# Kernel tuning notes

Measured on AMD Instinct MI355X. Metric: run time of the kernel, lower is better.

Reference implementation:

```python
import jax, jax.numpy as jnp
import numpy as np

B, S, E, H, L, DFF = 2, 2048, 512, 8, 2, 2048
D = E // H
EPS = 1e-5


def layernorm(x, g, b):
    mu = jnp.mean(x, axis=-1, keepdims=True)
    var = jnp.var(x, axis=-1, keepdims=True)
    return (x - mu) * jax.lax.rsqrt(var + EPS) * g + b


def layernorm_noaffine(x):
    mu = jnp.mean(x, axis=-1, keepdims=True)
    var = jnp.var(x, axis=-1, keepdims=True)
    return (x - mu) * jax.lax.rsqrt(var + EPS)


def setup_inputs() -> dict:
    key = jax.random.key(0)
    ks = jax.random.split(key, 16)
    s = 0.02
    inp = {
        "x": jax.random.normal(ks[0], (B, S, E), dtype=jnp.float32),
        "mask": jax.random.randint(ks[1], (B, S), 0, 2) == 1,
        # per-layer attention projections, stacked over layers
        "wq": jax.random.normal(ks[2], (L, E, E), dtype=jnp.float32) * s,
        "bq": jnp.zeros((L, E), dtype=jnp.float32),
        "wk": jax.random.normal(ks[3], (L, E, E), dtype=jnp.float32) * s,
        "bk": jnp.zeros((L, E), dtype=jnp.float32),
        "wv": jax.random.normal(ks[4], (L, E, E), dtype=jnp.float32) * s,
        "bv": jnp.zeros((L, E), dtype=jnp.float32),
        # shared norms (module defines a single norm1/norm2 used by every layer)
        "g1": jnp.ones((E,), dtype=jnp.float32),
        "b1": jnp.zeros((E,), dtype=jnp.float32),
        "g2": jnp.ones((E,), dtype=jnp.float32),
        "b2": jnp.zeros((E,), dtype=jnp.float32),
        "gf": jnp.ones((E,), dtype=jnp.float32),
        "bf": jnp.zeros((E,), dtype=jnp.float32),
        # shared Dense FFN (single self.dense used after every layer)
        "W1": jax.random.normal(ks[5], (DFF, E), dtype=jnp.float32) * s,
        "B1": jnp.zeros((DFF,), dtype=jnp.float32),
        "W2": jax.random.normal(ks[6], (E, DFF), dtype=jnp.float32) * s,
        "B2": jnp.zeros((E,), dtype=jnp.float32),
    }
    return inp


def _forward(x, wq, bq, wk, bk, wv, bv, g1, b1, g2, b2, gf, bf, W1, B1, W2, B2, mask):
    scale = 1.0 / jnp.sqrt(jnp.float32(D))
    m = mask[:, None, None, :]  # [B,1,1,S] key padding mask, True = pad
    neg_inf = jnp.float32(-jnp.inf)
    for i in range(L):
        h = layernorm(x, g1, b1)  # norm1(x), used for q,k,v
        q = (h @ wq[i].T + bq[i]).reshape(B, S, H, D).transpose(0, 2, 1, 3)
        k = (h @ wk[i].T + bk[i]).reshape(B, S, H, D).transpose(0, 2, 1, 3)
        v = (h @ wv[i].T + bv[i]).reshape(B, S, H, D).transpose(0, 2, 1, 3)
        logits = jnp.einsum("bhqd,bhkd->bhqk", q, k) * scale
        att = jax.nn.softmax(jnp.where(m, neg_inf, logits), axis=-1)
        att = jnp.where(m, 0.0, att)
        out = jnp.einsum("bhqk,bhkd->bhqd", att, v)
        out = out.transpose(0, 2, 1, 3).reshape(B, S, E)
        x = x + layernorm(out, g2, b2)
        # Dense: LayerNorm(no affine) -> Linear -> ReLU -> Linear, residual
        d = layernorm_noaffine(x)
        d = jax.nn.relu(d @ W1.T + B1)
        d = d @ W2.T + B2
        x = x + d
    return layernorm(x, gf, bf)


def reference(x, mask, wq, bq, wk, bk, wv, bv, g1, b1, g2, b2, gf, bf, W1, B1, W2, B2):
    return _forward(x, wq, bq, wk, bk, wv, bv, g1, b1, g2, b2, gf, bf, W1, B1, W2, B2, mask)
```

## Files before the change

kernel.cpp:

```cpp
#include <hip/hip_runtime.h>
#include <hip/hip_bf16.h>

constexpr int BB   = 2;
constexpr int SS   = 2048;
constexpr int EE   = 512;
constexpr int HH   = 8;
constexpr int DD   = 64;
constexpr int DFF_ = 2048;
constexpr int NTOK = BB * SS;
constexpr int NE   = NTOK * EE;
constexpr float EPSF  = 1e-5f;
constexpr float SCL2  = 0.125f * 1.44269504088896f;
constexpr float MBIAS = -1e30f;
constexpr int KSPLIT = 2;
constexpr int KHALF  = SS / KSPLIT;

typedef __bf16 v8bf __attribute__((ext_vector_type(8)));
typedef __bf16 v4bf __attribute__((ext_vector_type(4)));
typedef float  v4f  __attribute__((ext_vector_type(4)));

__device__ __forceinline__ float bf2f(unsigned short u) {
    return __uint_as_float(((unsigned int)u) << 16);
}
__device__ __forceinline__ float bf2f(__bf16 u) {
    unsigned short us = __builtin_bit_cast(unsigned short, u);
    return __uint_as_float(((unsigned int)us) << 16);
}
__device__ __forceinline__ float ldA(const void* p, size_t i, int f) {
    return f ? ((const float*)p)[i] : bf2f(((const unsigned short*)p)[i]);
}
__device__ __forceinline__ void gll16(const void* g, void* l) {
    __builtin_amdgcn_global_load_lds(
        (const __attribute__((address_space(1))) void*)g,
        (__attribute__((address_space(3))) void*)l, 16, 0, 0);
}

__global__ void sniff_kernel(const unsigned short* __restrict__ x, int* flag) {
    __shared__ int cnt[256];
    int t = threadIdx.x, bad = 0;
    for (int i = t; i < 4096; i += 256) {
        float v = bf2f(x[i]);
        if (!(fabsf(v) < 1000.f)) bad++;
    }
    cnt[t] = bad;
    __syncthreads();
    if (t == 0) {
        int s = 0;
        for (int i = 0; i < 256; ++i) s += cnt[i];
        *flag = (s > 8) ? 1 : 0;
    }
}

__global__ void cvt_kernel(const void* __restrict__ in, float* __restrict__ out,
                           int n, const int* __restrict__ flagp) {
    const int f = *flagp;
    int i = (blockIdx.x * blockDim.x + threadIdx.x) * 4;
    if (i >= n) return;
    if (f) {
        *(float4*)(out + i) = *(const float4*)((const float*)in + i);
    } else {
        ushort4 u = *(const ushort4*)((const unsigned short*)in + i);
        out[i + 0] = bf2f(u.x); out[i + 1] = bf2f(u.y);
        out[i + 2] = bf2f(u.z); out[i + 3] = bf2f(u.w);
    }
}

__global__ void wcvt_all(const void* __restrict__ wq, const void* __restrict__ wk,
                         const void* __restrict__ wv, const void* __restrict__ W1,
                         const void* __restrict__ W2, __bf16* __restrict__ out,
                         const int* __restrict__ flagp) {
    const int f = *flagp;
    const int i = (blockIdx.x * blockDim.x + threadIdx.x) * 8;
    constexpr int n1 = 2 * EE * EE;
    constexpr int nf = DFF_ * EE;
    const void* src; int off;
    if      (i < n1)          { src = wq; off = i; }
    else if (i < 2 * n1)      { src = wk; off = i - n1; }
    else if (i < 3 * n1)      { src = wv; off = i - 2 * n1; }
    else if (i < 3 * n1 + nf) { src = W1; off = i - 3 * n1; }
    else                      { src = W2; off = i - 3 * n1 - nf; }
    if (f) {
        const float* p = (const float*)src + off;
        #pragma unroll
        for (int j = 0; j < 8; ++j) out[i + j] = (__bf16)p[j];
    } else {
        *(uint4*)(out + i) = *(const uint4*)((const unsigned short*)src + off);
    }
}

__global__ __launch_bounds__(256) void ln_kernel(
    const float* __restrict__ src,
    const void* __restrict__ g, const void* __restrict__ b,
    __bf16* __restrict__ dstb, void* __restrict__ outp,
    const int* __restrict__ flagp)
{
    const int f = *flagp;
    const int row = blockIdx.x, t = threadIdx.x;
    const float* x = src + (size_t)row * EE;
    float v0 = x[t], v1 = x[t + 256];
    float s = v0 + v1, q = v0 * v0 + v1 * v1;
    #pragma unroll
    for (int off = 32; off > 0; off >>= 1) {
        s += __shfl_down(s, off, 64);
        q += __shfl_down(q, off, 64);
    }
    __shared__ float red[8], st[2];
    const int wid = t >> 6;
    if ((t & 63) == 0) { red[wid] = s; red[4 + wid] = q; }
    __syncthreads();
    if (t == 0) {
        float S_ = red[0] + red[1] + red[2] + red[3];
        float Q_ = red[4] + red[5] + red[6] + red[7];
        float mu = S_ / EE;
        st[0] = mu;
        st[1] = rsqrtf(Q_ / EE - mu * mu + EPSF);
    }
    __syncthreads();
    const float mu = st[0], rs = st[1];
    float o0 = (v0 - mu) * rs, o1 = (v1 - mu) * rs;
    if (g) {
        o0 = o0 * ldA(g, t, f)       + ldA(b, t, f);
        o1 = o1 * ldA(g, t + 256, f) + ldA(b, t + 256, f);
    }
    const size_t i0 = (size_t)row * EE + t, i1 = i0 + 256;
    if (dstb) { dstb[i0] = (__bf16)o0; dstb[i1] = (__bf16)o1; }
    if (outp) {
        if (f) { ((float*)outp)[i0] = o0; ((float*)outp)[i1] = o1; }
        else {
            ((__hip_bfloat16*)outp)[i0] = __float2bfloat16(o0);
            ((__hip_bfloat16*)outp)[i1] = __float2bfloat16(o1);
        }
    }
}

__global__ __launch_bounds__(256) void combine_ln(
    const __bf16* __restrict__ Opart, const float* __restrict__ MLl,
    const void* __restrict__ g2, const void* __restrict__ b2,
    float* __restrict__ X, __bf16* __restrict__ Hb,
    const int* __restrict__ flagp)
{
    const int f = *flagp;
    const int tok = blockIdx.x, t = threadIdx.x;
    const int b = tok >> 11, s_ = tok & 2047;
    __shared__ float cinv[8];
    __shared__ float red[8], st[2];
    if (t < 8) {
        float l = 0.f;
        #pragma unroll
        for (int zz = 0; zz < KSPLIT; ++zz)
            l += MLl[(size_t)(zz * 16 + b * 8 + t) * SS + s_];
        cinv[t] = (l > 0.f) ? 1.f / l : 0.f;
    }
    __syncthreads();
    float a0 = 0.f, a1 = 0.f;
    {
        int c = t, h = c >> 6, d = c & 63;
        #pragma unroll
        for (int zz = 0; zz < KSPLIT; ++zz)
            a0 += bf2f(Opart[((size_t)(zz * 16 + b * 8 + h) * SS + s_) * 64 + d]);
        a0 *= cinv[h];
        c = t + 256; h = c >> 6; d = c & 63;
        #pragma unroll
        for (int zz = 0; zz < KSPLIT; ++zz)
            a1 += bf2f(Opart[((size_t)(zz * 16 + b * 8 + h) * SS + s_) * 64 + d]);
        a1 *= cinv[h];
    }
    const int wid = t >> 6;
    {
        float s = a0 + a1, q = a0 * a0 + a1 * a1;
        #pragma unroll
        for (int off = 32; off > 0; off >>= 1) {
            s += __shfl_down(s, off, 64);
            q += __shfl_down(q, off, 64);
        }
        if ((t & 63) == 0) { red[wid] = s; red[4 + wid] = q; }
    }
    __syncthreads();
    if (t == 0) {
        float S_ = red[0] + red[1] + red[2] + red[3];
        float Q_ = red[4] + red[5] + red[6] + red[7];
        float mu = S_ / EE;
        st[0] = mu;
        st[1] = rsqrtf(Q_ / EE - mu * mu + EPSF);
    }
    __syncthreads();
    const float mu1 = st[0], rs1 = st[1];
    const size_t i0 = (size_t)tok * EE + t, i1 = i0 + 256;
    float l0v = (a0 - mu1) * rs1 * ldA(g2, t, f)       + ldA(b2, t, f);
    float l1v = (a1 - mu1) * rs1 * ldA(g2, t + 256, f) + ldA(b2, t + 256, f);
    float x0 = X[i0] + l0v, x1 = X[i1] + l1v;
    __syncthreads();
    {
        float s = x0 + x1, q = x0 * x0 + x1 * x1;
        #pragma unroll
        for (int off = 32; off > 0; off >>= 1) {
            s += __shfl_down(s, off, 64);
            q += __shfl_down(q, off, 64);
        }
        if ((t & 63) == 0) { red[wid] = s; red[4 + wid] = q; }
    }
    __syncthreads();
    if (t == 0) {
        float S_ = red[0] + red[1] + red[2] + red[3];
        float Q_ = red[4] + red[5] + red[6] + red[7];
        float mu = S_ / EE;
        st[0] = mu;
        st[1] = rsqrtf(Q_ / EE - mu * mu + EPSF);
    }
    __syncthreads();
    const float mu2 = st[0], rs2 = st[1];
    X[i0] = x0; X[i1] = x1;
    Hb[i0] = (__bf16)((x0 - mu2) * rs2);
    Hb[i1] = (__bf16)((x1 - mu2) * rs2);
}

__global__ __launch_bounds__(256) void gemm_mfma(
    const __bf16* __restrict__ A,
    const __bf16* Wa, const __bf16* Wb, const __bf16* Wc,
    const void* ba, const void* bb, const void* bc,
    __bf16* oa, __bf16* ob, __bf16* oc,
    float* __restrict__ Cf,
    int M, int N, int K, int flags,
    size_t welem_off, size_t belem_off, const int* __restrict__ flagp)
{
    const int f = *flagp;
    const int z = blockIdx.z;
    const __bf16* W = (z == 0) ? Wa : (z == 1) ? Wb : Wc;
    const void* bias = (z == 0) ? ba : (z == 1) ? bb : bc;
    __bf16* Cb = (z == 0) ? oa : (z == 1) ? ob : oc;
    W += welem_off;
    int kbeg = 0, kend = K;
    if (flags & 4) {
        const int ks = K >> 2;
        kbeg = z * ks; kend = kbeg + ks;
        if (z != 0) bias = nullptr;
    }

    __shared__ __bf16 As[2][128 * 32];
    __shared__ __bf16 Bs[2][128 * 32];
    const int t = threadIdx.x;
    const int w = t >> 6, lane = t & 63;
    const int quad = lane >> 4, l16 = lane & 15;
    const int wr = w >> 1, wc = w & 1;
    const int bm = blockIdx.x * 128, bn = blockIdx.y * 128;

    v4f acc[4][4] = {};
    const int c0 = t, c1 = t + 256;
    const int r0 = c0 >> 2, e0 = (c0 & 3) * 8;
    const int r1 = c1 >> 2, e1 = (c1 & 3) * 8;

    gll16(A + (size_t)(bm + r0) * K + kbeg + e0, (char*)As[0] + c0 * 16);
    gll16(A + (size_t)(bm + r1) * K + kbeg + e1, (char*)As[0] + c1 * 16);
    gll16(W + (size_t)(bn + r0) * K + kbeg + e0, (char*)Bs[0] + c0 * 16);
    gll16(W + (size_t)(bn + r1) * K + kbeg + e1, (char*)Bs[0] + c1 * 16);

    int p = 0;
    for (int k0 = kbeg; k0 < kend; k0 += 32) {
        __syncthreads();
        if (k0 + 32 < kend) {
            const int kn = k0 + 32, q_ = p ^ 1;
            gll16(A + (size_t)(bm + r0) * K + kn + e0, (char*)As[q_] + c0 * 16);
            gll16(A + (size_t)(bm + r1) * K + kn + e1, (char*)As[q_] + c1 * 16);
            gll16(W + (size_t)(bn + r0) * K + kn + e0, (char*)Bs[q_] + c0 * 16);
            gll16(W + (size_t)(bn + r1) * K + kn + e1, (char*)Bs[q_] + c1 * 16);
        }
        v8bf af[4], bfr[4];
        #pragma unroll
        for (int i = 0; i < 4; ++i) {
            int row = wr * 64 + i * 16 + l16;
            af[i] = *(const v8bf*)&As[p][row * 32 + quad * 8];
        }
        #pragma unroll
        for (int j = 0; j < 4; ++j) {
            int row = wc * 64 + j * 16 + l16;
            bfr[j] = *(const v8bf*)&Bs[p][row * 32 + quad * 8];
        }
        #pragma unroll
        for (int i = 0; i < 4; ++i)
            #pragma unroll
            for (int j = 0; j < 4; ++j)
                acc[i][j] = __builtin_amdgcn_mfma_f32_16x16x32_bf16(
                    af[i], bfr[j], acc[i][j], 0, 0, 0);
        p ^= 1;
    }

    float bvv[4];
    #pragma unroll
    for (int j = 0; j < 4; ++j) {
        int col = bn + wc * 64 + j * 16 + l16;
        bvv[j] = bias ? ldA(bias, belem_off + col, f) : 0.f;
    }

    if ((flags & 8) && z == 2) {
        #pragma unroll
        for (int i = 0; i < 4; ++i) {
            const int row0 = bm + wr * 64 + i * 16 + quad * 4;
            const int b_ = row0 >> 11, sl = row0 & 2047;
            const int s64 = sl & ~63, sloc = sl & 63;
            const int slot = (sloc & 32) + ((sloc >> 2) & 3) * 8 + ((sloc >> 4) & 1) * 4;
            #pragma unroll
            for (int j = 0; j < 4; ++j) {
                const int col = bn + wc * 64 + j * 16 + l16;
                const int h_ = col >> 6, d_ = col & 63;
                v4bf u;
                #pragma unroll
                for (int r = 0; r < 4; ++r) u[r] = (__bf16)(acc[i][j][r] + bvv[j]);
                *(v4bf*)(Cb + ((size_t)((b_ * 8 + h_) * 64 + d_)) * SS + s64 + slot) = u;
            }
        }
        return;
    }

    #pragma unroll
    for (int i = 0; i < 4; ++i) {
        const int rowb = bm + wr * 64 + i * 16 + quad * 4;
        #pragma unroll
        for (int j = 0; j < 4; ++j) {
            const int col = bn + wc * 64 + j * 16 + l16;
            #pragma unroll
            for (int r = 0; r < 4; ++r) {
                float v = acc[i][j][r] + bvv[j];
                if (flags & 1) v = fmaxf(v, 0.f);
                const size_t idx = (size_t)(rowb + r) * N + col;
                if (flags & 4)      unsafeAtomicAdd(&Cf[idx], v);
                else if (flags & 2) Cf[idx] += v;
                else                Cb[idx] = (__bf16)v;
            }
        }
    }
}

__global__ __launch_bounds__(512) void attn_mfma(
    const __bf16* __restrict__ Qg, const __bf16* __restrict__ Kg,
    const __bf16* __restrict__ Vtg, const int* __restrict__ mask,
    __bf16* __restrict__ Opart, float* __restrict__ MLl)
{
    __shared__ __bf16 Ks[64][72];
    __shared__ __bf16 Vs[64][72];
    __shared__ float  mkf[64];

    const int t = threadIdx.x;
    const int w = t >> 6, lane = t & 63;
    const int quad = lane >> 4, l16 = lane & 15;
    const int bh = blockIdx.y, b = bh >> 3, hh = bh & 7;
    const int q0 = blockIdx.x * 256;
    const int z  = blockIdx.z;
    const int kof = z * KHALF;

    const __bf16* qrow0 = Qg + ((size_t)(b * SS + q0 + w * 32 + l16)) * EE + hh * DD + quad * 8;
    const __bf16* qrow1 = qrow0 + (size_t)16 * EE;
    const v8bf qa00 = *(const v8bf*)qrow0;
    const v8bf qa01 = *(const v8bf*)(qrow0 + 32);
    const v8bf qa10 = *(const v8bf*)qrow1;
    const v8bf qa11 = *(const v8bf*)(qrow1 + 32);

    const int lr = t >> 3, lc = (t & 7) * 8;
    const __bf16* kbase = Kg  + ((size_t)(b * SS + kof + lr)) * EE + hh * DD + lc;
    const __bf16* vbase = Vtg + ((size_t)((b * 8 + hh) * 64 + lr)) * SS + kof + lc;

    v8bf ka = *(const v8bf*)kbase;
    v8bf va = *(const v8bf*)vbase;
    float mb = 0.f;
    if (t < 64) mb = mask[b * SS + kof + t] ? MBIAS : 0.f;

    float l0 = 0.f, l1 = 0.f;
    v4f o0[4] = {}, o1[4] = {};

    #pragma unroll 1
    for (int k0 = 0; k0 < KHALF; k0 += 64) {
        *(v8bf*)&Ks[lr][lc] = ka;
        *(v8bf*)&Vs[lr][lc] = va;
        if (t < 64) mkf[t] = mb;
        __syncthreads();
        if (k0 + 64 < KHALF) {
            ka = *(const v8bf*)(kbase + (size_t)(k0 + 64) * EE);
            va = *(const v8bf*)(vbase + (k0 + 64));
            if (t < 64) mb = mask[b * SS + kof + k0 + 64 + t] ? MBIAS : 0.f;
        }

        v4f s0[4], s1[4];
        #pragma unroll
        for (int j = 0; j < 4; ++j) {
            v8bf kf0 = *(const v8bf*)&Ks[j * 16 + l16][quad * 8];
            v8bf kf1 = *(const v8bf*)&Ks[j * 16 + l16][32 + quad * 8];
            v4f za = {}, zb = {};
            za = __builtin_amdgcn_mfma_f32_16x16x32_bf16(kf0, qa00, za, 0, 0, 0);
            za = __builtin_amdgcn_mfma_f32_16x16x32_bf16(kf1, qa01, za, 0, 0, 0);
            zb = __builtin_amdgcn_mfma_f32_16x16x32_bf16(kf0, qa10, zb, 0, 0, 0);
            zb = __builtin_amdgcn_mfma_f32_16x16x32_bf16(kf1, qa11, zb, 0, 0, 0);
            s0[j] = za; s1[j] = zb;
        }
        float4 mk4[4];
        #pragma unroll
        for (int j = 0; j < 4; ++j) mk4[j] = *(const float4*)&mkf[j * 16 + quad * 4];

        v8bf p00, p01, p10, p11;
        float t0 = 0.f, t1 = 0.f;
        #pragma unroll
        for (int j = 0; j < 4; ++j) {
            float a0 = exp2f(fmaf(s0[j][0], SCL2, mk4[j].x));
            float a1 = exp2f(fmaf(s0[j][1], SCL2, mk4[j].y));
            float a2 = exp2f(fmaf(s0[j][2], SCL2, mk4[j].z));
            float a3 = exp2f(fmaf(s0[j][3], SCL2, mk4[j].w));
            float b0 = exp2f(fmaf(s1[j][0], SCL2, mk4[j].x));
            float b1 = exp2f(fmaf(s1[j][1], SCL2, mk4[j].y));
            float b2 = exp2f(fmaf(s1[j][2], SCL2, mk4[j].z));
            float b3 = exp2f(fmaf(s1[j][3], SCL2, mk4[j].w));
            t0 += (a0 + a1) + (a2 + a3);
            t1 += (b0 + b1) + (b2 + b3);
            if (j < 2) {
                p00[j * 4 + 0] = (__bf16)a0; p00[j * 4 + 1] = (__bf16)a1;
                p00[j * 4 + 2] = (__bf16)a2; p00[j * 4 + 3] = (__bf16)a3;
                p10[j * 4 + 0] = (__bf16)b0; p10[j * 4 + 1] = (__bf16)b1;
                p10[j * 4 + 2] = (__bf16)b2; p10[j * 4 + 3] = (__bf16)b3;
            } else {
                p01[(j - 2) * 4 + 0] = (__bf16)a0; p01[(j - 2) * 4 + 1] = (__bf16)a1;
                p01[(j - 2) * 4 + 2] = (__bf16)a2; p01[(j - 2) * 4 + 3] = (__bf16)a3;
                p11[(j - 2) * 4 + 0] = (__bf16)b0; p11[(j - 2) * 4 + 1] = (__bf16)b1;
                p11[(j - 2) * 4 + 2] = (__bf16)b2; p11[(j - 2) * 4 + 3] = (__bf16)b3;
            }
        }
        l0 += t0; l1 += t1;

        #pragma unroll
        for (int dt = 0; dt < 4; ++dt) {
            v8bf vf0 = *(const v8bf*)&Vs[dt * 16 + l16][quad * 8];
            v8bf vf1 = *(const v8bf*)&Vs[dt * 16 + l16][32 + quad * 8];
            o0[dt] = __builtin_amdgcn_mfma_f32_16x16x32_bf16(vf0, p00, o0[dt], 0, 0, 0);
            o0[dt] = __builtin_amdgcn_mfma_f32_16x16x32_bf16(vf1, p01, o0[dt], 0, 0, 0);
            o1[dt] = __builtin_amdgcn_mfma_f32_16x16x32_bf16(vf0, p10, o1[dt], 0, 0, 0);
            o1[dt] = __builtin_amdgcn_mfma_f32_16x16x32_bf16(vf1, p11, o1[dt], 0, 0, 0);
        }
        __syncthreads();
    }

    l0 += __shfl_xor(l0, 16, 64);
    l0 += __shfl_xor(l0, 32, 64);
    l1 += __shfl_xor(l1, 16, 64);
    l1 += __shfl_xor(l1, 32, 64);

    const size_t qi0 = (size_t)(z * 16 + bh) * SS + (q0 + w * 32 + l16);
    const size_t qi1 = qi0 + 16;
    __bf16* op0 = Opart + qi0 * 64;
    __bf16* op1 = Opart + qi1 * 64;
    #pragma unroll
    for (int dt = 0; dt < 4; ++dt) {
        v4bf u0, u1;
        #pragma unroll
        for (int r = 0; r < 4; ++r) { u0[r] = (__bf16)o0[dt][r]; u1[r] = (__bf16)o1[dt][r]; }
        *(v4bf*)(op0 + dt * 16 + quad * 4) = u0;
        *(v4bf*)(op1 + dt * 16 + quad * 4) = u1;
    }
    if (quad == 0) { MLl[qi0] = l0; MLl[qi1] = l1; }
}

extern "C" void kernel_launch(void* const* d_in, const int* in_sizes, int n_in,
                              void* d_out, int out_size, void* d_ws, size_t ws_size,
                              hipStream_t stream) {
    const void* x_in = d_in[0];
    const int*  mask = (const int*)d_in[1];
    const void* wq = d_in[2];  const void* bq = d_in[3];
    const void* wk = d_in[4];  const void* bk = d_in[5];
    const void* wv = d_in[6];  const void* bv = d_in[7];
    const void* g1 = d_in[8];  const void* b1 = d_in[9];
    const void* g2 = d_in[10]; const void* b2 = d_in[11];
    const void* gf = d_in[12]; const void* bfp= d_in[13];
    const void* W1 = d_in[14]; const void* B1 = d_in[15];
    const void* W2 = d_in[16]; const void* B2 = d_in[17];

    float* base = (float*)d_ws;
    int*   flag = (int*)base;
    float* X   = base + 16;
    float* fQ  = X + NE;
    float* fK  = fQ + NE / 2;
    float* fV  = fK + NE / 2;
    float* fH  = fV + NE / 2;
    float* fW  = fH + NE / 2;
    __bf16* Qb    = (__bf16*)fQ;
    __bf16* Kb    = (__bf16*)fK;
    __bf16* Vtg   = (__bf16*)fV;
    __bf16* Hb    = (__bf16*)fH;
    __bf16* wqc = (__bf16*)fW;
    __bf16* wkc = wqc + 2 * EE * EE;
    __bf16* wvc = wkc + 2 * EE * EE;
    __bf16* W1c = wvc + 2 * EE * EE;
    __bf16* W2c = W1c + DFF_ * EE;
    float* MLl = (float*)(W2c + (size_t)EE * DFF_);
    float* fO  = MLl + (size_t)KSPLIT * 16 * SS;
    __bf16* Opart = (__bf16*)fO;
    __bf16* MID   = (__bf16*)fO;

    sniff_kernel<<<1, 256, 0, stream>>>((const unsigned short*)x_in, flag);
    cvt_kernel<<<NE / 4 / 256, 256, 0, stream>>>(x_in, X, NE, flag);
    wcvt_all<<<1792, 256, 0, stream>>>(wq, wk, wv, W1, W2, wqc, flag);

    const dim3 gQKV(NTOK / 128, EE / 128, 3);
    const dim3 gF1 (NTOK / 128, DFF_ / 128, 1);
    const dim3 gF2 (NTOK / 128, EE / 128, 4);
    const dim3 gAtt(SS / 256, BB * HH, KSPLIT);

    for (int l = 0; l < 2; ++l) {
        const size_t wo = (size_t)l * EE * EE, bo = (size_t)l * EE;
        ln_kernel<<<NTOK, 256, 0, stream>>>(X, g1, b1, Hb, nullptr, flag);
        gemm_mfma<<<gQKV, 256, 0, stream>>>(Hb, wqc, wkc, wvc, bq, bk, bv,
            Qb, Kb, Vtg, nullptr, NTOK, EE, EE, 8, wo, bo, flag);
        attn_mfma<<<gAtt, 512, 0, stream>>>(Qb, Kb, Vtg, mask, Opart, MLl);
        combine_ln<<<NTOK, 256, 0, stream>>>(Opart, MLl, g2, b2, X, Hb, flag);
        gemm_mfma<<<gF1, 256, 0, stream>>>(Hb, W1c, W1c, W1c, B1, B1, B1,
            MID, MID, MID, nullptr, NTOK, DFF_, EE, 1, 0, 0, flag);
        gemm_mfma<<<gF2, 256, 0, stream>>>(MID, W2c, W2c, W2c, B2, B2, B2,
            nullptr, nullptr, nullptr, X, NTOK, EE, DFF_, 2 | 4, 0, 0, flag);
    }
    ln_kernel<<<NTOK, 256, 0, stream>>>(X, gf, bfp, nullptr, d_out, flag);
}
```

Before: 362.0 us.

## Fuse input conversion with first layernorm and shrink attention blocks

```diff
diff --git a/kernel.cpp b/kernel.cpp
--- a/kernel.cpp
+++ b/kernel.cpp
@@ -51,18 +51,39 @@
     }
 }
 
-__global__ void cvt_kernel(const void* __restrict__ in, float* __restrict__ out,
-                           int n, const int* __restrict__ flagp) {
+__global__ __launch_bounds__(256) void cvt_ln(
+    const void* __restrict__ in, float* __restrict__ X,
+    const void* __restrict__ g, const void* __restrict__ b,
+    __bf16* __restrict__ Hb, const int* __restrict__ flagp)
+{
     const int f = *flagp;
-    int i = (blockIdx.x * blockDim.x + threadIdx.x) * 4;
-    if (i >= n) return;
-    if (f) {
-        *(float4*)(out + i) = *(const float4*)((const float*)in + i);
-    } else {
-        ushort4 u = *(const ushort4*)((const unsigned short*)in + i);
-        out[i + 0] = bf2f(u.x); out[i + 1] = bf2f(u.y);
-        out[i + 2] = bf2f(u.z); out[i + 3] = bf2f(u.w);
-    }
+    const int row = blockIdx.x, t = threadIdx.x;
+    const size_t i0 = (size_t)row * EE + t, i1 = i0 + 256;
+    float v0 = ldA(in, i0, f);
+    float v1 = ldA(in, i1, f);
+    float s = v0 + v1, q = v0 * v0 + v1 * v1;
+    #pragma unroll
+    for (int off = 32; off > 0; off >>= 1) {
+        s += __shfl_down(s, off, 64);
+        q += __shfl_down(q, off, 64);
+    }
+    __shared__ float red[8], st[2];
+    const int wid = t >> 6;
+    if ((t & 63) == 0) { red[wid] = s; red[4 + wid] = q; }
+    __syncthreads();
+    if (t == 0) {
+        float S_ = red[0] + red[1] + red[2] + red[3];
+        float Q_ = red[4] + red[5] + red[6] + red[7];
+        float mu = S_ / EE;
+        st[0] = mu;
+        st[1] = rsqrtf(Q_ / EE - mu * mu + EPSF);
+    }
+    __syncthreads();
+    const float mu = st[0], rs = st[1];
+    float o0 = (v0 - mu) * rs * ldA(g, t, f)       + ldA(b, t, f);
+    float o1 = (v1 - mu) * rs * ldA(g, t + 256, f) + ldA(b, t + 256, f);
+    X[i0] = v0; X[i1] = v1;
+    Hb[i0] = (__bf16)o0; Hb[i1] = (__bf16)o1;
 }
 
 __global__ void wcvt_all(const void* __restrict__ wq, const void* __restrict__ wk,
@@ -330,7 +351,7 @@
     }
 }
 
-__global__ __launch_bounds__(512) void attn_mfma(
+__global__ __launch_bounds__(256) void attn_mfma(
     const __bf16* __restrict__ Qg, const __bf16* __restrict__ Kg,
     const __bf16* __restrict__ Vtg, const int* __restrict__ mask,
     __bf16* __restrict__ Opart, float* __restrict__ MLl)
@@ -343,7 +364,7 @@
     const int w = t >> 6, lane = t & 63;
     const int quad = lane >> 4, l16 = lane & 15;
     const int bh = blockIdx.y, b = bh >> 3, hh = bh & 7;
-    const int q0 = blockIdx.x * 256;
+    const int q0 = blockIdx.x * 128;
     const int z  = blockIdx.z;
     const int kof = z * KHALF;
 
@@ -354,12 +375,12 @@
     const v8bf qa10 = *(const v8bf*)qrow1;
     const v8bf qa11 = *(const v8bf*)(qrow1 + 32);
 
-    const int lr = t >> 3, lc = (t & 7) * 8;
+    const int lr = t >> 2, lc = (t & 3) * 16;
     const __bf16* kbase = Kg  + ((size_t)(b * SS + kof + lr)) * EE + hh * DD + lc;
     const __bf16* vbase = Vtg + ((size_t)((b * 8 + hh) * 64 + lr)) * SS + kof + lc;
 
-    v8bf ka = *(const v8bf*)kbase;
-    v8bf va = *(const v8bf*)vbase;
+    v8bf ka0 = *(const v8bf*)kbase, ka1 = *(const v8bf*)(kbase + 8);
+    v8bf va0 = *(const v8bf*)vbase, va1 = *(const v8bf*)(vbase + 8);
     float mb = 0.f;
     if (t < 64) mb = mask[b * SS + kof + t] ? MBIAS : 0.f;
 
@@ -368,17 +389,22 @@
 
     #pragma unroll 1
     for (int k0 = 0; k0 < KHALF; k0 += 64) {
-        *(v8bf*)&Ks[lr][lc] = ka;
-        *(v8bf*)&Vs[lr][lc] = va;
+        *(v8bf*)&Ks[lr][lc]     = ka0;
+        *(v8bf*)&Ks[lr][lc + 8] = ka1;
+        *(v8bf*)&Vs[lr][lc]     = va0;
+        *(v8bf*)&Vs[lr][lc + 8] = va1;
         if (t < 64) mkf[t] = mb;
         __syncthreads();
         if (k0 + 64 < KHALF) {
-            ka = *(const v8bf*)(kbase + (size_t)(k0 + 64) * EE);
-            va = *(const v8bf*)(vbase + (k0 + 64));
+            ka0 = *(const v8bf*)(kbase + (size_t)(k0 + 64) * EE);
+            ka1 = *(const v8bf*)(kbase + (size_t)(k0 + 64) * EE + 8);
+            va0 = *(const v8bf*)(vbase + (k0 + 64));
+            va1 = *(const v8bf*)(vbase + (k0 + 64) + 8);
             if (t < 64) mb = mask[b * SS + kof + k0 + 64 + t] ? MBIAS : 0.f;
         }
 
         v4f s0[4], s1[4];
+        __builtin_amdgcn_s_setprio(1);
         #pragma unroll
         for (int j = 0; j < 4; ++j) {
             v8bf kf0 = *(const v8bf*)&Ks[j * 16 + l16][quad * 8];
@@ -390,6 +416,7 @@
             zb = __builtin_amdgcn_mfma_f32_16x16x32_bf16(kf1, qa11, zb, 0, 0, 0);
             s0[j] = za; s1[j] = zb;
         }
+        __builtin_amdgcn_s_setprio(0);
         float4 mk4[4];
         #pragma unroll
         for (int j = 0; j < 4; ++j) mk4[j] = *(const float4*)&mkf[j * 16 + quad * 4];
@@ -422,6 +449,7 @@
         }
         l0 += t0; l1 += t1;
 
+        __builtin_amdgcn_s_setprio(1);
         #pragma unroll
         for (int dt = 0; dt < 4; ++dt) {
             v8bf vf0 = *(const v8bf*)&Vs[dt * 16 + l16][quad * 8];
@@ -431,6 +459,7 @@
             o1[dt] = __builtin_amdgcn_mfma_f32_16x16x32_bf16(vf0, p10, o1[dt], 0, 0, 0);
             o1[dt] = __builtin_amdgcn_mfma_f32_16x16x32_bf16(vf1, p11, o1[dt], 0, 0, 0);
         }
+        __builtin_amdgcn_s_setprio(0);
         __syncthreads();
     }
 
@@ -491,20 +520,21 @@
     __bf16* MID   = (__bf16*)fO;
 
     sniff_kernel<<<1, 256, 0, stream>>>((const unsigned short*)x_in, flag);
-    cvt_kernel<<<NE / 4 / 256, 256, 0, stream>>>(x_in, X, NE, flag);
+    cvt_ln<<<NTOK, 256, 0, stream>>>(x_in, X, g1, b1, Hb, flag);
     wcvt_all<<<1792, 256, 0, stream>>>(wq, wk, wv, W1, W2, wqc, flag);
 
     const dim3 gQKV(NTOK / 128, EE / 128, 3);
     const dim3 gF1 (NTOK / 128, DFF_ / 128, 1);
     const dim3 gF2 (NTOK / 128, EE / 128, 4);
-    const dim3 gAtt(SS / 256, BB * HH, KSPLIT);
+    const dim3 gAtt(SS / 128, BB * HH, KSPLIT);
 
     for (int l = 0; l < 2; ++l) {
         const size_t wo = (size_t)l * EE * EE, bo = (size_t)l * EE;
-        ln_kernel<<<NTOK, 256, 0, stream>>>(X, g1, b1, Hb, nullptr, flag);
+        if (l > 0)
+            ln_kernel<<<NTOK, 256, 0, stream>>>(X, g1, b1, Hb, nullptr, flag);
         gemm_mfma<<<gQKV, 256, 0, stream>>>(Hb, wqc, wkc, wvc, bq, bk, bv,
             Qb, Kb, Vtg, nullptr, NTOK, EE, EE, 8, wo, bo, flag);
-        attn_mfma<<<gAtt, 512, 0, stream>>>(Qb, Kb, Vtg, mask, Opart, MLl);
+        attn_mfma<<<gAtt, 256, 0, stream>>>(Qb, Kb, Vtg, mask, Opart, MLl);
         combine_ln<<<NTOK, 256, 0, stream>>>(Opart, MLl, g2, b2, X, Hb, flag);
         gemm_mfma<<<gF1, 256, 0, stream>>>(Hb, W1c, W1c, W1c, B1, B1, B1,
             MID, MID, MID, nullptr, NTOK, DFF_, EE, 1, 0, 0, flag);
```

After: 365.7 us. About the same (+1.0%).
